# Kernel tuning notes

Measured on AMD Instinct MI355X. Metric: run time of the kernel, lower is better.

Reference implementation:

```python
import jax, jax.numpy as jnp
import numpy as np

BITS = 4
GROUPSIZE = 128
IN_FEATURES = 4096
OUT_FEATURES = 11008
N_GROUPS = IN_FEATURES // GROUPSIZE  # 32
MASK = (1 << BITS) - 1  # 15


def setup_inputs() -> dict:
    key = jax.random.key(0)
    ks = jax.random.split(key, 5)
    x = jax.random.normal(ks[0], (2, 2048, IN_FEATURES), dtype=jnp.float32)
    qweight = jax.random.randint(ks[1], (IN_FEATURES // 8, OUT_FEATURES), 0, 2**31 - 1, dtype=jnp.int32)
    qzeros = jax.random.randint(ks[2], (N_GROUPS, OUT_FEATURES // 8), 0, 2**31 - 1, dtype=jnp.int32)
    scales = jax.random.uniform(ks[3], (N_GROUPS, OUT_FEATURES), dtype=jnp.float16)
    bias = jax.random.normal(ks[4], (OUT_FEATURES,), dtype=jnp.float32)
    return {"x": x, "qweight": qweight, "qzeros": qzeros, "scales": scales, "bias": bias}


def _dequant(qweight, qzeros, scales):
    # wf = [0, 4, 8, ..., 28]: bit offsets of the 8 int4 nibbles in each int32
    wf = jnp.arange(0, 32, BITS, dtype=jnp.int32)
    # unpack weights: [IN//8, OUT] -> [IN//8, 8, OUT] -> [N_GROUPS, GROUPSIZE, OUT]
    w = (qweight[:, None, :] >> wf[None, :, None]) & MASK
    w = w.reshape(N_GROUPS, GROUPSIZE, OUT_FEATURES).astype(jnp.float32)
    # unpack zeros: [NG, OUT//8] -> [NG, OUT//8, 8] -> [NG, 1, OUT]
    z = (qzeros[:, :, None] >> wf[None, None, :]) & MASK
    z = z.reshape(N_GROUPS, 1, OUT_FEATURES).astype(jnp.float32)
    s = scales.astype(jnp.float32)[:, None, :]  # [NG, 1, OUT]
    # scales * w - scales * z, per group; fused elementwise
    return (s * (w - z)).reshape(IN_FEATURES, OUT_FEATURES)


def reference(x, qweight, qzeros, scales, bias):
    W = _dequant(qweight, qzeros, scales)  # [IN, OUT] fp32
    out = jnp.matmul(x.astype(jnp.float32), W) + bias
    return out
```

## Files before the change

kernel.cpp:

```cpp
#include <hip/hip_runtime.h>
#include <hip/hip_fp16.h>

#define K_DIM 4096
#define N_DIM 11008
#define NZ8   1376
#define BM    256
#define BN    256
#define NT_N  43
#define NKT   64
#define ATB   32768

typedef _Float16 f16x8 __attribute__((ext_vector_type(8)));
typedef float    f32x4 __attribute__((ext_vector_type(4)));

#define SB()    __builtin_amdgcn_sched_barrier(0)
#define BAR()   __builtin_amdgcn_s_barrier()
#define VMW(N)  do { asm volatile("s_waitcnt vmcnt(" #N ")" ::: "memory"); SB(); } while (0)
#define LGKM0() do { asm volatile("s_waitcnt lgkmcnt(0)" ::: "memory"); SB(); } while (0)

__device__ __forceinline__ f16x8 dq8(unsigned q, __half2 scp, __half2 nzp)
{
    const unsigned mu = 0xE400E400u;
    const __half2 m1024 = *(const __half2*)&mu;
    union { __half2 h2[4]; f16x8 v; } p;
#pragma unroll
    for (int d = 0; d < 4; ++d) {
        unsigned t = ((q >> (4 * d)) & 0x000F000Fu) | 0x64006400u;
        p.h2[d] = __hfma2(__hadd2(*(const __half2*)&t, m1024), scp, nzp);
    }
    return p.v;
}

__global__ __launch_bounds__(256)
void r15_xcvt(const float* __restrict__ x, __half* __restrict__ xh, int nchunks)
{
    int c = blockIdx.x * 256 + threadIdx.x;
    const int stride = gridDim.x * 256;
    for (; c < nchunks; c += stride) {
        const int row = c & 255;
        const int sl  = (c >> 8) & 3;
        const int kh  = (c >> 10) & 1;
        const int tl  = c >> 11;
        const int mt  = tl >> 6;
        const int kt  = tl & 63;
        const size_t gm = (size_t)mt * 256 + row;
        const int kb = kt * 64 + kh * 32 + sl * 8;
        const float4 f0 = *(const float4*)(x + gm * K_DIM + kb);
        const float4 f1 = *(const float4*)(x + gm * K_DIM + kb + 4);
        union { __half2 h2[4]; int4 v; } p;
        p.h2[0] = __floats2half2_rn(f0.x, f1.x);
        p.h2[1] = __floats2half2_rn(f0.y, f1.y);
        p.h2[2] = __floats2half2_rn(f0.z, f1.z);
        p.h2[3] = __floats2half2_rn(f0.w, f1.w);
        ((int4*)xh)[c] = p.v;
    }
}

#define ISSUE_Q8(D0,D1,D2,D3,D4,D5,D6,D7) do { \
    asm volatile( \
        "global_load_dword %0, %8, off\n\t" \
        "global_load_dword %1, %8, off offset:64\n\t" \
        "global_load_dword %2, %8, off offset:128\n\t" \
        "global_load_dword %3, %8, off offset:192\n\t" \
        "global_load_dword %4, %9, off\n\t" \
        "global_load_dword %5, %9, off offset:64\n\t" \
        "global_load_dword %6, %9, off offset:128\n\t" \
        "global_load_dword %7, %9, off offset:192" \
        : "=&v"(D0), "=&v"(D1), "=&v"(D2), "=&v"(D3), \
          "=&v"(D4), "=&v"(D5), "=&v"(D6), "=&v"(D7) \
        : "v"(qp0), "v"(qp1) : "memory"); \
    qp0 += 8 * N_DIM; qp1 += 8 * N_DIM; \
} while (0)

#define ISSUE_SZ() do { \
    asm volatile( \
        "global_load_dword %0, %8, off\n\t" \
        "global_load_dword %1, %8, off offset:64\n\t" \
        "global_load_dword %2, %8, off offset:128\n\t" \
        "global_load_dword %3, %8, off offset:192\n\t" \
        "global_load_dword %4, %9, off\n\t" \
        "global_load_dword %5, %9, off offset:8\n\t" \
        "global_load_dword %6, %9, off offset:16\n\t" \
        "global_load_dword %7, %9, off offset:24" \
        : "=&v"(sS0), "=&v"(sS1), "=&v"(sS2), "=&v"(sS3), \
          "=&v"(sZ0), "=&v"(sZ1), "=&v"(sZ2), "=&v"(sZ3) \
        : "v"(sp), "v"(zp) : "memory"); \
    sp += N_DIM; zp += NZ8; \
} while (0)

#define ISSUE_A(BUFP, T) do { \
    const char* _s = agp + (size_t)(T) * ATB; \
    _Pragma("unroll") for (int j = 0; j < 4; ++j) \
        __builtin_amdgcn_global_load_lds((const unsigned int*)(_s + j * 8192), \
            (unsigned int*)((BUFP) + j * 8192 + tid * 16), 16, 0, 0); \
} while (0)

#define FRAGS(ARp, KH) do { \
    _Pragma("unroll") for (int m = 0; m < 8; ++m) \
        af[m] = *(const f16x8*)((ARp) + (KH) * 16384 + aOff + m * 256); \
} while (0)

#define DQ4(Q0,Q1,Q2,Q3) do { \
    bf[0] = dq8(Q0, scp0, nzp0); bf[1] = dq8(Q1, scp1, nzp1); \
    bf[2] = dq8(Q2, scp2, nzp2); bf[3] = dq8(Q3, scp3, nzp3); \
} while (0)

#define MFMA32() do { \
    __builtin_amdgcn_s_setprio(1); \
    _Pragma("unroll") for (int m = 0; m < 8; ++m) \
        _Pragma("unroll") for (int n = 0; n < 4; ++n) \
            acc[m][n] = __builtin_amdgcn_mfma_f32_16x16x32_f16(af[m], bf[n], acc[m][n], 0, 0, 0); \
    __builtin_amdgcn_s_setprio(0); \
    SB(); \
} while (0)

#define CVT_S() do { \
    const float _s0 = __uint_as_float(sS0), _s1 = __uint_as_float(sS1); \
    const float _s2 = __uint_as_float(sS2), _s3 = __uint_as_float(sS3); \
    const __half _h0 = __float2half_rn(_s0), _h1 = __float2half_rn(_s1); \
    const __half _h2 = __float2half_rn(_s2), _h3 = __float2half_rn(_s3); \
    scp0 = __half2(_h0, _h0); scp1 = __half2(_h1, _h1); \
    scp2 = __half2(_h2, _h2); scp3 = __half2(_h3, _h3); \
    const __half _n0 = __float2half_rn(-_s0 * (float)((sZ0 >> sh4) & 15u)); \
    const __half _n1 = __float2half_rn(-_s1 * (float)((sZ1 >> sh4) & 15u)); \
    const __half _n2 = __float2half_rn(-_s2 * (float)((sZ2 >> sh4) & 15u)); \
    const __half _n3 = __float2half_rn(-_s3 * (float)((sZ3 >> sh4) & 15u)); \
    nzp0 = __half2(_n0, _n0); nzp1 = __half2(_n1, _n1); \
    nzp2 = __half2(_n2, _n2); nzp3 = __half2(_n3, _n3); \
} while (0)

__global__ __launch_bounds__(512, 2)
void r15_gemm(const __half* __restrict__ xh,
              const int*   __restrict__ qweight,
              const int*   __restrict__ qzeros,
              const float* __restrict__ scales,
              const float* __restrict__ bias,
              float* __restrict__ out)
{
    __shared__ __align__(16) unsigned char A0s[ATB], A1s[ATB];

    const int tid  = threadIdx.x;
    const int lane = tid & 63;
    const int wid  = tid >> 6;
    const int wr   = (wid >> 2) * 128;
    const int wc   = (wid & 3) * 64;

    int bid = blockIdx.x;
    const int cpx = gridDim.x >> 3;
    bid = (bid & 7) * cpx + (bid >> 3);
    const int bm0 = (bid / NT_N) * BM;
    const int bn0 = (bid % NT_N) * BN;

    const int frow = lane & 15, kb8 = lane >> 4;
    const int ngl2 = bn0 + wc + frow;
    const int sh4  = (ngl2 & 7) * 4;
    const int aOff = kb8 * 4096 + (wr + frow) * 16;

    const char* agp = (const char*)xh + ((size_t)(bm0 >> 8) * NKT) * ATB + tid * 16;

    const int*   qp0 = qweight + (size_t)kb8 * N_DIM + ngl2;
    const int*   qp1 = qweight + (size_t)(kb8 + 4) * N_DIM + ngl2;
    const float* sp  = scales + (size_t)N_DIM + ngl2;
    const int*   zp  = qzeros + (size_t)NZ8 + (ngl2 >> 3);

    unsigned char *aR = A0s, *aW = A1s;

    f32x4 acc[8][4];
#pragma unroll
    for (int m = 0; m < 8; ++m)
#pragma unroll
        for (int n = 0; n < 4; ++n)
            acc[m][n] = (f32x4){0.f, 0.f, 0.f, 0.f};
    f16x8 af[8], bf[4];
    __half2 scp0, scp1, scp2, scp3, nzp0, nzp1, nzp2, nzp3;
    unsigned qa0, qa1, qa2, qa3, qa4, qa5, qa6, qa7;
    unsigned qb0, qb1, qb2, qb3, qb4, qb5, qb6, qb7;
    unsigned sS0, sS1, sS2, sS3, sZ0, sZ1, sZ2, sZ3;

    sS0 = __float_as_uint(scales[ngl2]);
    sS1 = __float_as_uint(scales[ngl2 + 16]);
    sS2 = __float_as_uint(scales[ngl2 + 32]);
    sS3 = __float_as_uint(scales[ngl2 + 48]);
    sZ0 = (unsigned)qzeros[(ngl2 >> 3) + 0];
    sZ1 = (unsigned)qzeros[(ngl2 >> 3) + 2];
    sZ2 = (unsigned)qzeros[(ngl2 >> 3) + 4];
    sZ3 = (unsigned)qzeros[(ngl2 >> 3) + 6];
    asm volatile("" : "+v"(sS0), "+v"(sS1), "+v"(sS2), "+v"(sS3),
                      "+v"(sZ0), "+v"(sZ1), "+v"(sZ2), "+v"(sZ3));
    VMW(0);
    ISSUE_Q8(qa0, qa1, qa2, qa3, qa4, qa5, qa6, qa7);
    ISSUE_A(aR, 0);
    ISSUE_Q8(qb0, qb1, qb2, qb3, qb4, qb5, qb6, qb7);
    ISSUE_A(aW, 1);
    VMW(12);
    BAR();

    for (int u = 0; u < 31; ++u) {
        const int t0 = 2 * u;
        CVT_S();
        FRAGS(aR, 0); DQ4(qa0, qa1, qa2, qa3); LGKM0(); MFMA32();
        FRAGS(aR, 1); DQ4(qa4, qa5, qa6, qa7);
        ISSUE_Q8(qa0, qa1, qa2, qa3, qa4, qa5, qa6, qa7);
        ISSUE_SZ();
        LGKM0(); MFMA32();
        VMW(16);
        BAR(); SB();
        { unsigned char* tp = aR; aR = aW; aW = tp; }
        ISSUE_A(aW, t0 + 2);
        FRAGS(aR, 0); DQ4(qb0, qb1, qb2, qb3); LGKM0(); MFMA32();
        FRAGS(aR, 1); DQ4(qb4, qb5, qb6, qb7);
        ISSUE_Q8(qb0, qb1, qb2, qb3, qb4, qb5, qb6, qb7);
        LGKM0(); MFMA32();
        VMW(8);
        BAR(); SB();
        { unsigned char* tp = aR; aR = aW; aW = tp; }
        ISSUE_A(aW, t0 + 3);
    }

    CVT_S();
    FRAGS(aR, 0); DQ4(qa0, qa1, qa2, qa3); LGKM0(); MFMA32();
    FRAGS(aR, 1); DQ4(qa4, qa5, qa6, qa7); LGKM0(); MFMA32();
    VMW(0);
    BAR(); SB();
    { unsigned char* tp = aR; aR = aW; aW = tp; }
    FRAGS(aR, 0); DQ4(qb0, qb1, qb2, qb3); LGKM0(); MFMA32();
    FRAGS(aR, 1); DQ4(qb4, qb5, qb6, qb7); LGKM0(); MFMA32();

    const int crow0 = (lane >> 4) << 2, ccol = lane & 15;
#pragma unroll
    for (int n = 0; n < 4; ++n) {
        const int col = bn0 + wc + n * 16 + ccol;
        const float bv = bias[col];
#pragma unroll
        for (int m = 0; m < 8; ++m) {
            const int row = bm0 + wr + m * 16 + crow0;
#pragma unroll
            for (int j = 0; j < 4; ++j)
                out[(size_t)(row + j) * N_DIM + col] = acc[m][n][j] + bv;
        }
    }
}

typedef __bf16 bf16x8 __attribute__((ext_vector_type(8)));

__global__ __launch_bounds__(256, 2)
void r15_fb(const float* __restrict__ x,
            const int*   __restrict__ qweight,
            const int*   __restrict__ qzeros,
            const float* __restrict__ scales,
            const float* __restrict__ bias,
            float* __restrict__ out)
{
    __shared__ __align__(16) unsigned char Asm[128 * 64 * 2];
    __shared__ __align__(16) unsigned char Bsm[128 * 64 * 2];
    const int tid = threadIdx.x, lane = tid & 63, wv = tid >> 6;
    const int wr = (wv >> 1) * 64, wc = (wv & 1) * 64;
    int bid = blockIdx.x;
    const int cpx = gridDim.x >> 3;
    bid = (bid & 7) * cpx + (bid >> 3);
    const int bm0 = (bid / 86) * 128, bn0 = (bid % 86) * 128;
    const int ar = tid >> 4, ac4 = tid & 15;
    const float* xp = x + (size_t)(bm0 + ar) * K_DIM + ac4 * 4;
    unsigned char* aw = Asm + ar * 128 + ((ac4 * 8) ^ ((ar & 7) << 4));
    const int bnn = tid & 127, bk8q = tid >> 7, ngl = bn0 + bnn;
    const int* qwp = qweight + (size_t)bk8q * N_DIM + ngl;
    unsigned char* bw = Bsm + bnn * 128;
    const int bsw = bnn & 7;
    const int frow = lane & 15, kb8 = lane >> 4, fsw = frow & 7;
    f32x4 acc[4][4];
#pragma unroll
    for (int m = 0; m < 4; ++m)
#pragma unroll
        for (int n = 0; n < 4; ++n) acc[m][n] = (f32x4){0.f, 0.f, 0.f, 0.f};
    float sc = 0.f, nsz = 0.f;
    for (int kt = 0; kt < K_DIM / 64; ++kt) {
        const int k0 = kt * 64;
        if ((k0 & 127) == 0) {
            const int g = k0 >> 7;
            sc = scales[(size_t)g * N_DIM + ngl];
            const unsigned zq = (unsigned)qzeros[(size_t)g * NZ8 + (ngl >> 3)];
            nsz = -sc * (float)((zq >> ((ngl & 7) * 4)) & 15u);
        }
#pragma unroll
        for (int i = 0; i < 8; ++i) {
            const float4 v = *(const float4*)(xp + (size_t)i * 16 * K_DIM + k0);
            union { __bf16 h[4]; unsigned long long u; } p;
            p.h[0] = (__bf16)v.x; p.h[1] = (__bf16)v.y;
            p.h[2] = (__bf16)v.z; p.h[3] = (__bf16)v.w;
            *(unsigned long long*)(aw + i * 16 * 128) = p.u;
        }
#pragma unroll
        for (int i = 0; i < 4; ++i) {
            const int k8 = 2 * i + bk8q;
            const unsigned q = (unsigned)qwp[(size_t)(kt * 8 + 2 * i) * N_DIM];
            union { __bf16 h[8]; bf16x8 v8; } p;
#pragma unroll
            for (int j = 0; j < 8; ++j)
                p.h[j] = (__bf16)__builtin_fmaf(sc, (float)((q >> (4 * j)) & 15u), nsz);
            *(bf16x8*)(bw + ((k8 ^ bsw) << 4)) = p.v8;
        }
        __syncthreads();
#pragma unroll
        for (int kh = 0; kh < 2; ++kh) {
            const int ksl = (kh << 2) + kb8;
            bf16x8 a2[4], b2[4];
#pragma unroll
            for (int m = 0; m < 4; ++m)
                a2[m] = *(const bf16x8*)(Asm + (wr + m * 16 + frow) * 128 + ((ksl ^ fsw) << 4));
#pragma unroll
            for (int n = 0; n < 4; ++n)
                b2[n] = *(const bf16x8*)(Bsm + (wc + n * 16 + frow) * 128 + ((ksl ^ fsw) << 4));
#pragma unroll
            for (int m = 0; m < 4; ++m)
#pragma unroll
                for (int n = 0; n < 4; ++n)
                    acc[m][n] = __builtin_amdgcn_mfma_f32_16x16x32_bf16(a2[m], b2[n], acc[m][n], 0, 0, 0);
        }
        __syncthreads();
    }
    const int crow0 = (lane >> 4) << 2, ccol = lane & 15;
#pragma unroll
    for (int n = 0; n < 4; ++n) {
        const int col = bn0 + wc + n * 16 + ccol;
        const float bv = bias[col];
#pragma unroll
        for (int m = 0; m < 4; ++m) {
            const int row = bm0 + wr + m * 16 + crow0;
#pragma unroll
            for (int j = 0; j < 4; ++j)
                out[(size_t)(row + j) * N_DIM + col] = acc[m][n][j] + bv;
        }
    }
}

extern "C" void kernel_launch(void* const* d_in, const int* in_sizes, int n_in,
                              void* d_out, int out_size, void* d_ws, size_t ws_size,
                              hipStream_t stream)
{
    const float* x   = (const float*)d_in[0];
    const int*   qw  = (const int*)d_in[1];
    const int*   qz  = (const int*)d_in[2];
    const float* scl = (const float*)d_in[3];
    const float* bs  = (const float*)d_in[4];
    float* out = (float*)d_out;

    const int M = in_sizes[0] / K_DIM;
    const size_t xh_bytes = (size_t)M * K_DIM * 2;

    if (ws_size >= xh_bytes) {
        __half* xh = (__half*)d_ws;
        const int nchunks = M * K_DIM / 8;
        hipLaunchKernelGGL(r15_xcvt, dim3(2048), dim3(256), 0, stream, x, xh, nchunks);
        dim3 grid((M / BM) * NT_N);
        hipLaunchKernelGGL(r15_gemm, grid, dim3(512), 0, stream,
                           xh, qw, qz, scl, bs, out);
    } else {
        dim3 grid((M / 128) * 86);
        hipLaunchKernelGGL(r15_fb, grid, dim3(256), 0, stream,
                           x, qw, qz, scl, bs, out);
    }
}
```

Baseline: 386.2 us.

## Pre-dequantize weights to fp16 tiles and run plain fp16 GEMM

Adds a separate kernel that dequantizes the int4 weights into a tiled fp16 workspace. A new GEMM then streams both A and B tiles into LDS through global_load_lds with double buffering, 256 threads and a 256x256 tile. This removes the per-tile dequant ALU work and the register pressure of the fused kernel. The cost is an extra pass that writes about 90 MB of fp16 weights and reads them back, plus a larger workspace requirement, falling back to the fused path when the workspace is too small.

```diff
diff --git a/kernel.cpp b/kernel.cpp
--- a/kernel.cpp
+++ b/kernel.cpp
@@ -4,19 +4,17 @@
 #define K_DIM 4096
 #define N_DIM 11008
 #define NZ8   1376
-#define BM    256
-#define BN    256
-#define NT_N  43
 #define NKT   64
+#define NT_N2 43
 #define ATB   32768
+#define XH_BYTES  33554432ull
+#define WT_BYTES  90177536ull
 
 typedef _Float16 f16x8 __attribute__((ext_vector_type(8)));
 typedef float    f32x4 __attribute__((ext_vector_type(4)));
 
 #define SB()    __builtin_amdgcn_sched_barrier(0)
-#define BAR()   __builtin_amdgcn_s_barrier()
 #define VMW(N)  do { asm volatile("s_waitcnt vmcnt(" #N ")" ::: "memory"); SB(); } while (0)
-#define LGKM0() do { asm volatile("s_waitcnt lgkmcnt(0)" ::: "memory"); SB(); } while (0)
 
 __device__ __forceinline__ f16x8 dq8(unsigned q, __half2 scp, __half2 nzp)
 {
@@ -32,7 +30,7 @@
 }
 
 __global__ __launch_bounds__(256)
-void r15_xcvt(const float* __restrict__ x, __half* __restrict__ xh, int nchunks)
+void r22_xcvt(const float* __restrict__ x, __half* __restrict__ xh, int nchunks)
 {
     int c = blockIdx.x * 256 + threadIdx.x;
     const int stride = gridDim.x * 256;
@@ -56,6 +54,125 @@
     }
 }
 
+__global__ __launch_bounds__(256)
+void r22_wcvt(const int* __restrict__ qweight, const int* __restrict__ qzeros,
+              const float* __restrict__ scales, __half* __restrict__ wt, int nchunks)
+{
+    int c = blockIdx.x * 256 + threadIdx.x;
+    const int stride = gridDim.x * 256;
+    for (; c < nchunks; c += stride) {
+        const int nl = c & 255;
+        const int sl = (c >> 8) & 3;
+        const int kh = (c >> 10) & 1;
+        const int kt = (c >> 11) & 63;
+        const int nt = c >> 17;
+        const int n  = nt * 256 + nl;
+        const int g  = kt >> 1;
+        const unsigned q = (unsigned)qweight[(size_t)(kt * 8 + kh * 4 + sl) * N_DIM + n];
+        const float s = scales[(size_t)g * N_DIM + n];
+        const unsigned zq = (unsigned)qzeros[(size_t)g * NZ8 + (n >> 3)];
+        const float zf = (float)((zq >> ((n & 7) * 4)) & 15u);
+        const __half sh = __float2half_rn(s), nh = __float2half_rn(-s * zf);
+        const f16x8 v = dq8(q, __half2(sh, sh), __half2(nh, nh));
+        *(f16x8*)(wt + (size_t)c * 8) = v;
+    }
+}
+
+__global__ __launch_bounds__(256, 1)
+void r22_gemm(const __half* __restrict__ xh,
+              const __half* __restrict__ wt,
+              const float* __restrict__ bias,
+              float* __restrict__ out)
+{
+    __shared__ __align__(16) unsigned char Ab[2][ATB];
+    __shared__ __align__(16) unsigned char Bb[2][ATB];
+
+    const int tid  = threadIdx.x;
+    const int lane = tid & 63;
+    const int wid  = tid >> 6;
+    const int wr   = (wid >> 1) * 128;
+    const int wc   = (wid & 1) * 128;
+
+    int bid = blockIdx.x;
+    const int cpx = gridDim.x >> 3;
+    bid = (bid & 7) * cpx + (bid >> 3);
+    const int mt = bid / NT_N2;
+    const int nt = bid % NT_N2;
+
+    const int frow = lane & 15, kb8 = lane >> 4;
+    const int aOff = kb8 * 4096 + (wr + frow) * 16;
+    const int bOff = kb8 * 4096 + (wc + frow) * 16;
+
+    const char* agp = (const char*)xh + (size_t)mt * NKT * ATB + tid * 16;
+    const char* bgp = (const char*)wt + (size_t)nt * NKT * ATB + tid * 16;
+
+    f32x4 acc[8][8];
+#pragma unroll
+    for (int m = 0; m < 8; ++m)
+#pragma unroll
+        for (int n = 0; n < 8; ++n)
+            acc[m][n] = (f32x4){0.f, 0.f, 0.f, 0.f};
+
+#pragma unroll
+    for (int j = 0; j < 8; ++j) {
+        __builtin_amdgcn_global_load_lds((const unsigned int*)(agp + j * 4096),
+            (unsigned int*)&Ab[0][j * 4096 + tid * 16], 16, 0, 0);
+        __builtin_amdgcn_global_load_lds((const unsigned int*)(bgp + j * 4096),
+            (unsigned int*)&Bb[0][j * 4096 + tid * 16], 16, 0, 0);
+    }
+    __syncthreads();
+
+    for (int t = 0; t < NKT; ++t) {
+        const int cur = t & 1;
+        if (t + 1 < NKT) {
+            const char* an = agp + (size_t)(t + 1) * ATB;
+            const char* bn = bgp + (size_t)(t + 1) * ATB;
+#pragma unroll
+            for (int j = 0; j < 8; ++j) {
+                __builtin_amdgcn_global_load_lds((const unsigned int*)(an + j * 4096),
+                    (unsigned int*)&Ab[cur ^ 1][j * 4096 + tid * 16], 16, 0, 0);
+                __builtin_amdgcn_global_load_lds((const unsigned int*)(bn + j * 4096),
+                    (unsigned int*)&Bb[cur ^ 1][j * 4096 + tid * 16], 16, 0, 0);
+            }
+        }
+        const unsigned char* Ac = &Ab[cur][0];
+        const unsigned char* Bc = &Bb[cur][0];
+#pragma unroll
+        for (int kh = 0; kh < 2; ++kh) {
+            f16x8 af[8], bf[8];
+#pragma unroll
+            for (int m = 0; m < 8; ++m)
+                af[m] = *(const f16x8*)(Ac + kh * 16384 + aOff + m * 256);
+#pragma unroll
+            for (int n = 0; n < 8; ++n)
+                bf[n] = *(const f16x8*)(Bc + kh * 16384 + bOff + n * 256);
+            __builtin_amdgcn_s_setprio(1);
+#pragma unroll
+            for (int m = 0; m < 8; ++m)
+#pragma unroll
+                for (int n = 0; n < 8; ++n)
+                    acc[m][n] = __builtin_amdgcn_mfma_f32_16x16x32_f16(
+                        af[m], bf[n], acc[m][n], 0, 0, 0);
+            __builtin_amdgcn_s_setprio(0);
+        }
+        __syncthreads();
+    }
+
+    const int crow0 = (lane >> 4) << 2, ccol = lane & 15;
+#pragma unroll
+    for (int n = 0; n < 8; ++n) {
+        const int col = nt * 256 + wc + n * 16 + ccol;
+        const float bv = bias[col];
+#pragma unroll
+        for (int m = 0; m < 8; ++m) {
+            const int row = mt * 256 + wr + m * 16 + crow0;
+#pragma unroll
+            for (int j = 0; j < 4; ++j)
+                out[(size_t)(row + j) * N_DIM + col] = acc[m][n][j] + bv;
+        }
+    }
+}
+
 #define ISSUE_Q8(D0,D1,D2,D3,D4,D5,D6,D7) do { \
     asm volatile( \
         "global_load_dword %0, %8, off\n\t" \
@@ -130,12 +247,12 @@
 } while (0)
 
 __global__ __launch_bounds__(512, 2)
-void r15_gemm(const __half* __restrict__ xh,
-              const int*   __restrict__ qweight,
-              const int*   __restrict__ qzeros,
-              const float* __restrict__ scales,
-              const float* __restrict__ bias,
-              float* __restrict__ out)
+void r22_fused(const __half* __restrict__ xh,
+               const int*   __restrict__ qweight,
+               const int*   __restrict__ qzeros,
+               const float* __restrict__ scales,
+               const float* __restrict__ bias,
+               float* __restrict__ out)
 {
     __shared__ __align__(16) unsigned char A0s[ATB], A1s[ATB];
 
@@ -148,8 +265,8 @@
     int bid = blockIdx.x;
     const int cpx = gridDim.x >> 3;
     bid = (bid & 7) * cpx + (bid >> 3);
-    const int bm0 = (bid / NT_N) * BM;
-    const int bn0 = (bid % NT_N) * BN;
+    const int bm0 = (bid / NT_N2) * 256;
+    const int bn0 = (bid % NT_N2) * 256;
 
     const int frow = lane & 15, kb8 = lane >> 4;
     const int ngl2 = bn0 + wc + frow;
@@ -193,38 +310,52 @@
     ISSUE_Q8(qb0, qb1, qb2, qb3, qb4, qb5, qb6, qb7);
     ISSUE_A(aW, 1);
     VMW(12);
-    BAR();
+    __builtin_amdgcn_s_barrier();
 
     for (int u = 0; u < 31; ++u) {
         const int t0 = 2 * u;
         CVT_S();
-        FRAGS(aR, 0); DQ4(qa0, qa1, qa2, qa3); LGKM0(); MFMA32();
+        FRAGS(aR, 0); DQ4(qa0, qa1, qa2, qa3);
+        asm volatile("s_waitcnt lgkmcnt(0)" ::: "memory"); SB();
+        MFMA32();
         FRAGS(aR, 1); DQ4(qa4, qa5, qa6, qa7);
         ISSUE_Q8(qa0, qa1, qa2, qa3, qa4, qa5, qa6, qa7);
         ISSUE_SZ();
-        LGKM0(); MFMA32();
+        asm volatile("s_waitcnt lgkmcnt(0)" ::: "memory"); SB();
+        MFMA32();
         VMW(16);
-        BAR(); SB();
+        __builtin_amdgcn_s_barrier(); SB();
         { unsigned char* tp = aR; aR = aW; aW = tp; }
         ISSUE_A(aW, t0 + 2);
-        FRAGS(aR, 0); DQ4(qb0, qb1, qb2, qb3); LGKM0(); MFMA32();
+        FRAGS(aR, 0); DQ4(qb0, qb1, qb2, qb3);
+        asm volatile("s_waitcnt lgkmcnt(0)" ::: "memory"); SB();
+        MFMA32();
         FRAGS(aR, 1); DQ4(qb4, qb5, qb6, qb7);
         ISSUE_Q8(qb0, qb1, qb2, qb3, qb4, qb5, qb6, qb7);
-        LGKM0(); MFMA32();
+        asm volatile("s_waitcnt lgkmcnt(0)" ::: "memory"); SB();
+        MFMA32();
         VMW(8);
-        BAR(); SB();
+        __builtin_amdgcn_s_barrier(); SB();
         { unsigned char* tp = aR; aR = aW; aW = tp; }
         ISSUE_A(aW, t0 + 3);
     }
 
     CVT_S();
-    FRAGS(aR, 0); DQ4(qa0, qa1, qa2, qa3); LGKM0(); MFMA32();
-    FRAGS(aR, 1); DQ4(qa4, qa5, qa6, qa7); LGKM0(); MFMA32();
+    FRAGS(aR, 0); DQ4(qa0, qa1, qa2, qa3);
+    asm volatile("s_waitcnt lgkmcnt(0)" ::: "memory"); SB();
+    MFMA32();
+    FRAGS(aR, 1); DQ4(qa4, qa5, qa6, qa7);
+    asm volatile("s_waitcnt lgkmcnt(0)" ::: "memory"); SB();
+    MFMA32();
     VMW(0);
-    BAR(); SB();
+    __builtin_amdgcn_s_barrier(); SB();
     { unsigned char* tp = aR; aR = aW; aW = tp; }
-    FRAGS(aR, 0); DQ4(qb0, qb1, qb2, qb3); LGKM0(); MFMA32();
-    FRAGS(aR, 1); DQ4(qb4, qb5, qb6, qb7); LGKM0(); MFMA32();
+    FRAGS(aR, 0); DQ4(qb0, qb1, qb2, qb3);
+    asm volatile("s_waitcnt lgkmcnt(0)" ::: "memory"); SB();
+    MFMA32();
+    FRAGS(aR, 1); DQ4(qb4, qb5, qb6, qb7);
+    asm volatile("s_waitcnt lgkmcnt(0)" ::: "memory"); SB();
+    MFMA32();
 
     const int crow0 = (lane >> 4) << 2, ccol = lane & 15;
 #pragma unroll
@@ -233,98 +364,6 @@
         const float bv = bias[col];
 #pragma unroll
         for (int m = 0; m < 8; ++m) {
-            const int row = bm0 + wr + m * 16 + crow0;
-#pragma unroll
-            for (int j = 0; j < 4; ++j)
-                out[(size_t)(row + j) * N_DIM + col] = acc[m][n][j] + bv;
-        }
-    }
-}
-
-typedef __bf16 bf16x8 __attribute__((ext_vector_type(8)));
-
-__global__ __launch_bounds__(256, 2)
-void r15_fb(const float* __restrict__ x,
-            const int*   __restrict__ qweight,
-            const int*   __restrict__ qzeros,
-            const float* __restrict__ scales,
-            const float* __restrict__ bias,
-            float* __restrict__ out)
-{
-    __shared__ __align__(16) unsigned char Asm[128 * 64 * 2];
-    __shared__ __align__(16) unsigned char Bsm[128 * 64 * 2];
-    const int tid = threadIdx.x, lane = tid & 63, wv = tid >> 6;
-    const int wr = (wv >> 1) * 64, wc = (wv & 1) * 64;
-    int bid = blockIdx.x;
-    const int cpx = gridDim.x >> 3;
-    bid = (bid & 7) * cpx + (bid >> 3);
-    const int bm0 = (bid / 86) * 128, bn0 = (bid % 86) * 128;
-    const int ar = tid >> 4, ac4 = tid & 15;
-    const float* xp = x + (size_t)(bm0 + ar) * K_DIM + ac4 * 4;
-    unsigned char* aw = Asm + ar * 128 + ((ac4 * 8) ^ ((ar & 7) << 4));
-    const int bnn = tid & 127, bk8q = tid >> 7, ngl = bn0 + bnn;
-    const int* qwp = qweight + (size_t)bk8q * N_DIM + ngl;
-    unsigned char* bw = Bsm + bnn * 128;
-    const int bsw = bnn & 7;
-    const int frow = lane & 15, kb8 = lane >> 4, fsw = frow & 7;
-    f32x4 acc[4][4];
-#pragma unroll
-    for (int m = 0; m < 4; ++m)
-#pragma unroll
-        for (int n = 0; n < 4; ++n) acc[m][n] = (f32x4){0.f, 0.f, 0.f, 0.f};
-    float sc = 0.f, nsz = 0.f;
-    for (int kt = 0; kt < K_DIM / 64; ++kt) {
-        const int k0 = kt * 64;
-        if ((k0 & 127) == 0) {
-            const int g = k0 >> 7;
-            sc = scales[(size_t)g * N_DIM + ngl];
-            const unsigned zq = (unsigned)qzeros[(size_t)g * NZ8 + (ngl >> 3)];
-            nsz = -sc * (float)((zq >> ((ngl & 7) * 4)) & 15u);
-        }
-#pragma unroll
-        for (int i = 0; i < 8; ++i) {
-            const float4 v = *(const float4*)(xp + (size_t)i * 16 * K_DIM + k0);
-            union { __bf16 h[4]; unsigned long long u; } p;
-            p.h[0] = (__bf16)v.x; p.h[1] = (__bf16)v.y;
-            p.h[2] = (__bf16)v.z; p.h[3] = (__bf16)v.w;
-            *(unsigned long long*)(aw + i * 16 * 128) = p.u;
-        }
-#pragma unroll
-        for (int i = 0; i < 4; ++i) {
-            const int k8 = 2 * i + bk8q;
-            const unsigned q = (unsigned)qwp[(size_t)(kt * 8 + 2 * i) * N_DIM];
-            union { __bf16 h[8]; bf16x8 v8; } p;
-#pragma unroll
-            for (int j = 0; j < 8; ++j)
-                p.h[j] = (__bf16)__builtin_fmaf(sc, (float)((q >> (4 * j)) & 15u), nsz);
-            *(bf16x8*)(bw + ((k8 ^ bsw) << 4)) = p.v8;
-        }
-        __syncthreads();
-#pragma unroll
-        for (int kh = 0; kh < 2; ++kh) {
-            const int ksl = (kh << 2) + kb8;
-            bf16x8 a2[4], b2[4];
-#pragma unroll
-            for (int m = 0; m < 4; ++m)
-                a2[m] = *(const bf16x8*)(Asm + (wr + m * 16 + frow) * 128 + ((ksl ^ fsw) << 4));
-#pragma unroll
-            for (int n = 0; n < 4; ++n)
-                b2[n] = *(const bf16x8*)(Bsm + (wc + n * 16 + frow) * 128 + ((ksl ^ fsw) << 4));
-#pragma unroll
-            for (int m = 0; m < 4; ++m)
-#pragma unroll
-                for (int n = 0; n < 4; ++n)
-                    acc[m][n] = __builtin_amdgcn_mfma_f32_16x16x32_bf16(a2[m], b2[n], acc[m][n], 0, 0, 0);
-        }
-        __syncthreads();
-    }
-    const int crow0 = (lane >> 4) << 2, ccol = lane & 15;
-#pragma unroll
-    for (int n = 0; n < 4; ++n) {
-        const int col = bn0 + wc + n * 16 + ccol;
-        const float bv = bias[col];
-#pragma unroll
-        for (int m = 0; m < 4; ++m) {
             const int row = bm0 + wr + m * 16 + crow0;
 #pragma unroll
             for (int j = 0; j < 4; ++j)
@@ -345,18 +384,22 @@
     float* out = (float*)d_out;
 
     const int M = in_sizes[0] / K_DIM;
-    const size_t xh_bytes = (size_t)M * K_DIM * 2;
-
-    if (ws_size >= xh_bytes) {
+    const int na = M * K_DIM / 8;
+
+    if (ws_size >= XH_BYTES + WT_BYTES) {
         __half* xh = (__half*)d_ws;
-        const int nchunks = M * K_DIM / 8;
-        hipLaunchKernelGGL(r15_xcvt, dim3(2048), dim3(256), 0, stream, x, xh, nchunks);
-        dim3 grid((M / BM) * NT_N);
-        hipLaunchKernelGGL(r15_gemm, grid, dim3(512), 0, stream,
+        __half* wt = (__half*)((char*)d_ws + XH_BYTES);
+        hipLaunchKernelGGL(r22_xcvt, dim3(2048), dim3(256), 0, stream, x, xh, na);
+        hipLaunchKernelGGL(r22_wcvt, dim3(2048), dim3(256), 0, stream,
+                           qw, qz, scl, wt, (int)(WT_BYTES / 16));
+        dim3 grid((M / 256) * NT_N2);
+        hipLaunchKernelGGL(r22_gemm, grid, dim3(256), 0, stream,
+                           xh, wt, bs, out);
+    } else {
+        __half* xh = (__half*)d_ws;
+        hipLaunchKernelGGL(r22_xcvt, dim3(2048), dim3(256), 0, stream, x, xh, na);
+        dim3 grid((M / 256) * NT_N2);
+        hipLaunchKernelGGL(r22_fused, grid, dim3(512), 0, stream,
                            xh, qw, qz, scl, bs, out);
-    } else {
-        dim3 grid((M / 128) * 86);
-        hipLaunchKernelGGL(r15_fb, grid, dim3(256), 0, stream,
-                           x, qw, qz, scl, bs, out);
-    }
-}
+    }
+}
```

New measurement: 515.9 us. 33.6% more time.
